# Kernel tuning notes

Measured on AMD Instinct MI355X. Metric: run time of the kernel, lower is better.

Reference implementation:

```python
import jax, jax.numpy as jnp
import numpy as np

NUM_HEADS = 8

def _qkv(t, W, b, H):
    # t: [B, L, C] -> q, k, v each [B, H, L, D]
    B, L, C = t.shape
    D = C // H
    qkv = (t @ W + b).reshape(B, L, 3, H, D)
    qkv = jnp.moveaxis(qkv, 2, 0)           # [3, B, L, H, D]
    qkv = jnp.swapaxes(qkv, 2, 3)           # [3, B, H, L, D]
    return qkv[0], qkv[1], qkv[2]

def _attend(q, k, v, scale):
    # q,k,v: [B, H, L, D] -> [B, L, C]
    B, H, L, D = q.shape
    scores = jnp.einsum('bhqd,bhkd->bhqk', q, k) * scale
    attn = jax.nn.softmax(scores, axis=-1)
    out = jnp.einsum('bhqk,bhkd->bhqd', attn, v)
    return jnp.swapaxes(out, 1, 2).reshape(B, L, H * D)

def setup_inputs() -> dict:
    key = jax.random.key(0)
    ks = jax.random.split(key, 7)
    B, N, C = 8, 2048, 512
    s_in = 1.0 / np.sqrt(C)
    return {
        'x': jax.random.normal(ks[0], (B, N, C), dtype=jnp.float32),
        'W_rgb_qkv': jax.random.normal(ks[1], (C, 3 * C), dtype=jnp.float32) * s_in,
        'b_rgb_qkv': jax.random.normal(ks[2], (3 * C,), dtype=jnp.float32) * 0.02,
        'W_depth_qkv': jax.random.normal(ks[3], (C, 3 * C), dtype=jnp.float32) * s_in,
        'b_depth_qkv': jax.random.normal(ks[4], (3 * C,), dtype=jnp.float32) * 0.02,
        'W_proj': jax.random.normal(ks[5], (C, C), dtype=jnp.float32) * s_in,
        'b_proj': jax.random.normal(ks[6], (C,), dtype=jnp.float32) * 0.02,
    }

def reference(x, W_rgb_qkv, b_rgb_qkv, W_depth_qkv, b_depth_qkv, W_proj, b_proj):
    B, N, C = x.shape
    H = NUM_HEADS
    D = C // H
    scale = D ** -0.5
    L = N // 2
    rgb, depth = x[:, :L], x[:, L:]
    rq, rk, rv = _qkv(rgb, W_rgb_qkv, b_rgb_qkv, H)
    dq, dk, dv = _qkv(depth, W_depth_qkv, b_depth_qkv, H)
    # rgb queries attend to depth K/V (named depth_v in torch code)
    depth_out = _attend(rq, dk, dv, scale)
    # depth queries attend to rgb K/V (named rgb_v in torch code)
    rgb_out = _attend(dq, rk, rv, scale)
    out = jnp.concatenate([rgb_out, depth_out], axis=1)  # [B, N, C]
    return out @ W_proj + b_proj
```

## Files before the change

kernel.cpp:

```cpp
#include <hip/hip_runtime.h>
#include <hip/hip_bf16.h>

typedef __attribute__((ext_vector_type(8))) short s16x8;
typedef __attribute__((ext_vector_type(4))) float f32x4;

__device__ __forceinline__ ushort f2bf(float f) {
  union { float f; unsigned int u; } c; c.f = f;
  unsigned int u = c.u + 0x7fffu + ((c.u >> 16) & 1u);
  return (ushort)(u >> 16);
}

__device__ __forceinline__ unsigned int pack2(float lo, float hi) {
  __hip_bfloat162 b2 = __float22bfloat162_rn(make_float2(lo, hi));
  union { __hip_bfloat162 b; unsigned int u; } c; c.b = b2;
  return c.u;
}

__device__ __forceinline__ s16x8 ld16(const ushort* p) {
  union { uint4 u; s16x8 s; } c;
  c.u = *reinterpret_cast<const uint4*>(p);
  return c.s;
}

__device__ __forceinline__ f32x4 mfma16(s16x8 a, s16x8 b, f32x4 c) {
  return __builtin_amdgcn_mfma_f32_16x16x32_bf16(a, b, c, 0, 0, 0);
}

__device__ __forceinline__ float exp2fast(float x) { return __builtin_amdgcn_exp2f(x); }

__device__ __forceinline__ void gld_lds16(const void* g, void* l) {
  __builtin_amdgcn_global_load_lds(
      (const __attribute__((address_space(1))) void*)g,
      (__attribute__((address_space(3))) void*)l, 16, 0, 0);
}


__global__ __launch_bounds__(256) void k_prep(
    const float* __restrict__ x, ushort* __restrict__ xb,
    const float* __restrict__ Wr, ushort* __restrict__ WtR,
    const float* __restrict__ Wd, ushort* __restrict__ WtD,
    const float* __restrict__ Wp, ushort* __restrict__ WtP) {
  __shared__ float tile[32][33];
  int b = blockIdx.x, t = threadIdx.x;
  if (b < 8192) {
    int i = (b * 256 + t) * 4;
    float4 v = *reinterpret_cast<const float4*>(x + i);
    ushort4 o;
    o.x = f2bf(v.x); o.y = f2bf(v.y); o.z = f2bf(v.z); o.w = f2bf(v.w);
    *reinterpret_cast<ushort4*>(xb + i) = o;
    return;
  }
  b -= 8192;
  const float* src; ushort* dst; int N;
  if (b < 768)      { src = Wr; dst = WtR; N = 1536; }
  else if (b < 1536){ b -= 768;  src = Wd; dst = WtD; N = 1536; }
  else              { b -= 1536; src = Wp; dst = WtP; N = 512; }
  int nb = N >> 5;
  int n0 = (b % nb) * 32, k0 = (b / nb) * 32;
  int tx = t & 31, ty = t >> 5;
#pragma unroll
  for (int i = 0; i < 32; i += 8)
    tile[ty + i][tx] = src[(k0 + ty + i) * N + (n0 + tx)];
  __syncthreads();
#pragma unroll
  for (int i = 0; i < 32; i += 8)
    dst[(size_t)(n0 + ty + i) * 512 + (k0 + tx)] = f2bf(tile[tx][ty + i]);
}


__device__ __forceinline__ s16x8 lds_frag(const char* lds, int row, int c) {
  union { uint4 u; s16x8 s; } cv;
  cv.u = *reinterpret_cast<const uint4*>(lds + row * 128 + ((c ^ (row & 7)) * 16));
  return cv.s;
}

__device__ __forceinline__ s16x8 lds_frag32(const char* lds, int row, int c) {
  union { uint4 u; s16x8 s; } cv;
  cv.u = *reinterpret_cast<const uint4*>(lds + row * 64 + ((c ^ ((row >> 1) & 3)) * 16));
  return cv.s;
}

__device__ __forceinline__ void stage_lds(const ushort* __restrict__ src, int ld,
                                          char* ldsbase, int t) {
#pragma unroll
  for (int p = 0; p < 4; ++p) {
    int chunk = p * 256 + t;
    int r = chunk >> 3, cc = chunk & 7;
    gld_lds16(src + r * ld + ((cc ^ (r & 7)) * 8), ldsbase + (chunk & ~63) * 16);
  }
}


template <bool TRANS>
__global__ __launch_bounds__(256) void k_qkv(
    const ushort* __restrict__ xb, const ushort* __restrict__ WtR,
    const ushort* __restrict__ WtD, const float* __restrict__ bR,
    const float* __restrict__ bD, ushort* __restrict__ Qb,
    ushort* __restrict__ Kb, ushort* __restrict__ Vt) {
  __shared__ __align__(16) char lds[49152];
  int m0 = blockIdx.x * 128;
  int n0 = (TRANS ? 1024 : 0) + blockIdx.y * 128;
  int s = m0 >> 13, bb = (m0 >> 10) & 7, lbase = m0 & 1023;
  const ushort* A = xb + (size_t)(bb * 2048 + s * 1024 + lbase) * 512;
  const ushort* Wt = (s ? WtD : WtR) + (size_t)n0 * 512;
  const float* bias = s ? bD : bR;
  int t = threadIdx.x;
  int wid = t >> 6, ln = t & 15, g = (t & 63) >> 4;
  int wr = wid >> 1, wc = wid & 1;

  int r0 = t >> 2, c0 = t & 3;
  int r1 = (t + 256) >> 2, c1 = t & 3;
  int so0 = r0 * 512 + ((c0 ^ ((r0 >> 1) & 3)) * 8);
  int so1 = r1 * 512 + ((c1 ^ ((r1 >> 1) & 3)) * 8);
  int ldu = (t & ~63) * 16;

  const ushort* As = A;
  const ushort* Bs = Wt;
  char* b0 = lds;
  char* b1 = lds + 16384;
  char* b2 = lds + 32768;

  f32x4 acc[4][4] = {};

  gld_lds16(As + so0, b0 + ldu);
  gld_lds16(As + so1, b0 + 4096 + ldu);
  gld_lds16(Bs + so0, b0 + 8192 + ldu);
  gld_lds16(Bs + so1, b0 + 12288 + ldu);
  As += 32; Bs += 32;
  gld_lds16(As + so0, b1 + ldu);
  gld_lds16(As + so1, b1 + 4096 + ldu);
  gld_lds16(Bs + so0, b1 + 8192 + ldu);
  gld_lds16(Bs + so1, b1 + 12288 + ldu);
  As += 32; Bs += 32;
  asm volatile("s_waitcnt vmcnt(4)" ::: "memory");
  __builtin_amdgcn_sched_barrier(0);
  __builtin_amdgcn_s_barrier();
  __builtin_amdgcn_sched_barrier(0);

  for (int ks = 0; ks < 16; ++ks) {
    if (ks < 14) {
      gld_lds16(As + so0, b2 + ldu);
      gld_lds16(As + so1, b2 + 4096 + ldu);
      gld_lds16(Bs + so0, b2 + 8192 + ldu);
      gld_lds16(Bs + so1, b2 + 12288 + ldu);
      As += 32; Bs += 32;
    }
    s16x8 af[4], bf[4];
    __builtin_amdgcn_s_setprio(1);
#pragma unroll
    for (int mi = 0; mi < 4; ++mi) af[mi] = lds_frag32(b0, wr * 64 + mi * 16 + ln, g);
#pragma unroll
    for (int ni = 0; ni < 4; ++ni) bf[ni] = lds_frag32(b0 + 8192, wc * 64 + ni * 16 + ln, g);
#pragma unroll
    for (int mi = 0; mi < 4; ++mi)
#pragma unroll
      for (int ni = 0; ni < 4; ++ni)
        acc[mi][ni] = TRANS ? mfma16(bf[ni], af[mi], acc[mi][ni])
                            : mfma16(af[mi], bf[ni], acc[mi][ni]);
    __builtin_amdgcn_s_setprio(0);

    if (ks < 15) {
      if (ks < 14) {
        asm volatile("s_waitcnt vmcnt(4)" ::: "memory");
      } else {
        asm volatile("s_waitcnt vmcnt(0)" ::: "memory");
      }
      __builtin_amdgcn_sched_barrier(0);
      __builtin_amdgcn_s_barrier();
      __builtin_amdgcn_sched_barrier(0);
    }
    char* tmp = b0; b0 = b1; b1 = b2; b2 = tmp;
  }

  int hb_base = (s * 8 + bb) * 8;
  if (!TRANS) {
    bool isK = (n0 >> 9) != 0;
    ushort* dst = isK ? Kb : Qb;
    float sc = isK ? 1.0f : 0.18033688011112042f;
#pragma unroll
    for (int mi = 0; mi < 4; ++mi)
#pragma unroll
      for (int ni = 0; ni < 4; ++ni) {
        f32x4 v = acc[mi][ni];
        int col = n0 + wc * 64 + ni * 16 + ln;
        int h = (col >> 6) & 7, d = col & 63;
        float bv = bias[col];
        ushort* hp = dst + ((size_t)(hb_base + h) << 16);
        int lr = lbase + wr * 64 + mi * 16 + g * 4;
#pragma unroll
        for (int j = 0; j < 4; ++j) hp[(lr + j) * 64 + d] = f2bf((v[j] + bv) * sc);
      }
  } else {
    __syncthreads();
    ushort* et = (ushort*)lds;
#pragma unroll
    for (int mi = 0; mi < 4; ++mi) {
      int ll = wr * 64 + mi * 16 + ln;
      int lpl = (ll & ~63) | (ll & 0x23) | ((ll & 0x0C) << 1) | ((ll & 0x10) >> 2);
      int chunk = lpl >> 3, within = lpl & 7;
#pragma unroll
      for (int ni = 0; ni < 4; ++ni) {
        f32x4 v = acc[mi][ni];
        int crb = wc * 64 + ni * 16 + g * 4;
#pragma unroll
        for (int j = 0; j < 4; ++j) {
          int cr = crb + j;
          float bv = bias[n0 + cr];
          *(ushort*)((char*)et + cr * 256 + ((chunk ^ (cr & 15)) * 16) + within * 2)
              = f2bf(v[j] + bv);
        }
      }
    }
    __syncthreads();
#pragma unroll
    for (int pass = 0; pass < 8; ++pass) {
      int rrow = pass * 16 + (t >> 4);
      int c16 = t & 15;
      int col = n0 + rrow;
      int h = (col >> 6) & 7, d = col & 63;
      uint4 vv = *(const uint4*)((const char*)et + rrow * 256 + ((c16 ^ (rrow & 15)) * 16));
      *reinterpret_cast<uint4*>(Vt + ((size_t)(hb_base + h) << 16) + d * 1024 + lbase + c16 * 8)
          = vv;
    }
  }
}


__global__ __launch_bounds__(512) void k_attn(const ushort* __restrict__ Qb,
                                              const ushort* __restrict__ Kb,
                                              const ushort* __restrict__ Vt,
                                              ushort* __restrict__ AO) {
  __shared__ __align__(16) char lds[32768];
  int bid = blockIdx.x;
  int set = bid & 127, qb = bid >> 7;
  int pair = set & 1, h = (set >> 1) & 7, bb = set >> 4;
  int sQ = 1 - pair, sKV = pair;
  const ushort* Qp = Qb + ((size_t)((sQ * 8 + bb) * 8 + h) << 16);
  const ushort* Kp = Kb + ((size_t)((sKV * 8 + bb) * 8 + h) << 16);
  const ushort* Vp = Vt + ((size_t)((sKV * 8 + bb) * 8 + h) << 16);
  int t = threadIdx.x, w = t >> 6, ln = t & 15, g = (t & 63) >> 4;
  int q0 = qb * 128 + w * 16;
  s16x8 qf0 = ld16(Qp + (q0 + ln) * 64 + g * 8);
  s16x8 qf1 = ld16(Qp + (q0 + ln) * 64 + 32 + g * 8);

  int r = t >> 3, cc = t & 7;
  int kof = r * 64 + ((cc ^ (r & 7)) * 8);
  int vof = r * 1024 + ((cc ^ (r & 7)) * 8);
  int ldst = (t & ~63) * 16;

  float ls = 0.f;
  f32x4 oc[4] = {};

  const ushort* kstage = Kp;
  const ushort* vstage = Vp;

  char* bc = lds;
  char* bn = lds + 16384;

  gld_lds16(kstage + kof, bc + ldst);
  gld_lds16(vstage + vof, bc + 8192 + ldst);
  kstage += 4096; vstage += 64;
  asm volatile("s_waitcnt vmcnt(0)" ::: "memory");
  __builtin_amdgcn_sched_barrier(0);
  __builtin_amdgcn_s_barrier();
  __builtin_amdgcn_sched_barrier(0);

  for (int it = 0; it < 16; ++it) {
    if (it < 15) {
      gld_lds16(kstage + kof, bn + ldst);
      gld_lds16(vstage + vof, bn + 8192 + ldst);
      kstage += 4096; vstage += 64;
    }

    f32x4 z[4];
    __builtin_amdgcn_s_setprio(1);
#pragma unroll
    for (int s = 0; s < 4; ++s) {
      s16x8 k0 = lds_frag(bc, s * 16 + ln, g);
      s16x8 k1 = lds_frag(bc, s * 16 + ln, 4 + g);
      f32x4 z1 = {}; z1 = mfma16(k0, qf0, z1); z1 = mfma16(k1, qf1, z1); z[s] = z1;
    }
    __builtin_amdgcn_s_setprio(0);

    unsigned int pw[8];
#pragma unroll
    for (int s = 0; s < 4; ++s) {
      float p0 = exp2fast(z[s][0]), p1 = exp2fast(z[s][1]);
      float p2 = exp2fast(z[s][2]), p3 = exp2fast(z[s][3]);
      ls += (p0 + p1) + (p2 + p3);
      pw[2 * s] = pack2(p0, p1); pw[2 * s + 1] = pack2(p2, p3);
    }
    union { uint4 u; s16x8 v; } c0, c1;
    c0.u = make_uint4(pw[0], pw[1], pw[2], pw[3]);
    c1.u = make_uint4(pw[4], pw[5], pw[6], pw[7]);
    s16x8 pf0 = c0.v, pf1 = c1.v;

    __builtin_amdgcn_s_setprio(1);
#pragma unroll
    for (int d = 0; d < 4; ++d) {
      s16x8 v0 = lds_frag(bc + 8192, d * 16 + ln, g);
      s16x8 v1 = lds_frag(bc + 8192, d * 16 + ln, 4 + g);
      oc[d] = mfma16(v0, pf0, oc[d]);
      oc[d] = mfma16(v1, pf1, oc[d]);
    }
    __builtin_amdgcn_s_setprio(0);

    if (it < 15) {
      asm volatile("s_waitcnt vmcnt(0)" ::: "memory");
      __builtin_amdgcn_sched_barrier(0);
      __builtin_amdgcn_s_barrier();
      __builtin_amdgcn_sched_barrier(0);
    }
    char* tmp = bc; bc = bn; bn = tmp;
  }

  ls += __shfl_xor(ls, 16, 64);
  ls += __shfl_xor(ls, 32, 64);
  float inv = 1.0f / ls;
  int orow = bb * 2048 + pair * 1024 + q0 + ln;
#pragma unroll
  for (int d = 0; d < 4; ++d) {
    uint2 st;
    st.x = pack2(oc[d][0] * inv, oc[d][1] * inv);
    st.y = pack2(oc[d][2] * inv, oc[d][3] * inv);
    *reinterpret_cast<uint2*>(AO + (size_t)orow * 512 + h * 64 + d * 16 + 4 * g) = st;
  }
}


__global__ __launch_bounds__(256) void k_gemm_proj(const ushort* __restrict__ AO,
                                                   const ushort* __restrict__ WtP,
                                                   const float* __restrict__ bP,
                                                   float* __restrict__ Out) {
  __shared__ __align__(16) char lds[65536];
  int m0 = blockIdx.x * 128, n0 = blockIdx.y * 128;
  const ushort* A = AO + (size_t)m0 * 512;
  const ushort* Wt = WtP + (size_t)n0 * 512;
  int t = threadIdx.x;
  int wid = t >> 6, ln = t & 15, g = (t & 63) >> 4;
  int wr = wid >> 1, wc = wid & 1;
  f32x4 acc[4][4] = {};
  stage_lds(A, 512, lds, t);
  stage_lds(Wt, 512, lds + 16384, t);
  __syncthreads();
  for (int ks = 0; ks < 8; ++ks) {
    char* cbuf = lds + (ks & 1) * 32768;
    if (ks < 7) {
      char* nbuf = lds + ((ks + 1) & 1) * 32768;
      stage_lds(A + (ks + 1) * 64, 512, nbuf, t);
      stage_lds(Wt + (ks + 1) * 64, 512, nbuf + 16384, t);
    }
    char* ldsA = cbuf;
    char* ldsB = cbuf + 16384;
#pragma unroll
    for (int kk = 0; kk < 2; ++kk) {
      s16x8 af[4], bf[4];
#pragma unroll
      for (int mi = 0; mi < 4; ++mi) af[mi] = lds_frag(ldsA, wr * 64 + mi * 16 + ln, kk * 4 + g);
#pragma unroll
      for (int ni = 0; ni < 4; ++ni) bf[ni] = lds_frag(ldsB, wc * 64 + ni * 16 + ln, kk * 4 + g);
#pragma unroll
      for (int mi = 0; mi < 4; ++mi)
#pragma unroll
        for (int ni = 0; ni < 4; ++ni) acc[mi][ni] = mfma16(af[mi], bf[ni], acc[mi][ni]);
    }
    __syncthreads();
  }
#pragma unroll
  for (int mi = 0; mi < 4; ++mi)
#pragma unroll
    for (int ni = 0; ni < 4; ++ni) {
      f32x4 v = acc[mi][ni];
      int col = n0 + wc * 64 + ni * 16 + ln;
      float bv = bP[col];
      int r0 = m0 + wr * 64 + mi * 16 + g * 4;
#pragma unroll
      for (int j = 0; j < 4; ++j) Out[(size_t)(r0 + j) * 512 + col] = v[j] + bv;
    }
}


extern "C" void kernel_launch(void* const* d_in, const int* in_sizes, int n_in,
                              void* d_out, int out_size, void* d_ws, size_t ws_size,
                              hipStream_t stream) {
  const float* x      = (const float*)d_in[0];
  const float* W_rgb  = (const float*)d_in[1];
  const float* b_rgb  = (const float*)d_in[2];
  const float* W_dep  = (const float*)d_in[3];
  const float* b_dep  = (const float*)d_in[4];
  const float* W_proj = (const float*)d_in[5];
  const float* b_proj = (const float*)d_in[6];
  float* out = (float*)d_out;

  char* ws = (char*)d_ws;
  ushort* xb  = (ushort*)(ws + 0);
  ushort* WtR = (ushort*)(ws + 16777216);
  ushort* WtD = (ushort*)(ws + 18350080);
  ushort* WtP = (ushort*)(ws + 19922944);
  ushort* Qb  = (ushort*)(ws + 20447232);
  ushort* Kb  = (ushort*)(ws + 37224448);
  ushort* Vt  = (ushort*)(ws + 54001664);
  ushort* AO  = (ushort*)(ws + 70778880);

  k_prep<<<9984, 256, 0, stream>>>(x, xb, W_rgb, WtR, W_dep, WtD, W_proj, WtP);
  k_qkv<false><<<dim3(128, 8), 256, 0, stream>>>(xb, WtR, WtD, b_rgb, b_dep, Qb, Kb, Vt);
  k_qkv<true><<<dim3(128, 4), 256, 0, stream>>>(xb, WtR, WtD, b_rgb, b_dep, Qb, Kb, Vt);
  k_attn<<<1024, 512, 0, stream>>>(Qb, Kb, Vt, AO);
  k_gemm_proj<<<dim3(128, 4), 256, 0, stream>>>(AO, WtP, b_proj, out);
}
```

Before: 131.6 us.

## Process two 16-row query tiles per wave in attention kernel with half the threads

The attention kernel now launches 256 threads per block instead of 512, and each wave handles 32 query rows as two 16-row MFMA tiles. Each K and V fragment read from LDS is reused for both tiles, and each thread issues two global-to-LDS loads per matrix to cover the 64-row staging tile. The goal is to halve LDS fragment traffic per query row and amortize staging and barrier overhead across more MFMA work. In exchange, register use per thread roughly doubles and there are fewer waves per block, which could reduce latency hiding.

```diff
diff --git a/kernel.cpp b/kernel.cpp
--- a/kernel.cpp
+++ b/kernel.cpp
@@ -226,7 +226,7 @@
 }
 
 
-__global__ __launch_bounds__(512) void k_attn(const ushort* __restrict__ Qb,
+__global__ __launch_bounds__(256) void k_attn(const ushort* __restrict__ Qb,
                                               const ushort* __restrict__ Kb,
                                               const ushort* __restrict__ Vt,
                                               ushort* __restrict__ AO) {
@@ -239,17 +239,22 @@
   const ushort* Kp = Kb + ((size_t)((sKV * 8 + bb) * 8 + h) << 16);
   const ushort* Vp = Vt + ((size_t)((sKV * 8 + bb) * 8 + h) << 16);
   int t = threadIdx.x, w = t >> 6, ln = t & 15, g = (t & 63) >> 4;
-  int q0 = qb * 128 + w * 16;
-  s16x8 qf0 = ld16(Qp + (q0 + ln) * 64 + g * 8);
-  s16x8 qf1 = ld16(Qp + (q0 + ln) * 64 + 32 + g * 8);
-
-  int r = t >> 3, cc = t & 7;
-  int kof = r * 64 + ((cc ^ (r & 7)) * 8);
-  int vof = r * 1024 + ((cc ^ (r & 7)) * 8);
+  int q0 = qb * 128 + w * 32;
+  s16x8 qf0a = ld16(Qp + (q0 + ln) * 64 + g * 8);
+  s16x8 qf1a = ld16(Qp + (q0 + ln) * 64 + 32 + g * 8);
+  s16x8 qf0b = ld16(Qp + (q0 + 16 + ln) * 64 + g * 8);
+  s16x8 qf1b = ld16(Qp + (q0 + 16 + ln) * 64 + 32 + g * 8);
+
+  int rA = t >> 3, ccA = t & 7;
+  int rB = 32 + (t >> 3), ccB = t & 7;
+  int kofA = rA * 64 + ((ccA ^ (rA & 7)) * 8);
+  int kofB = rB * 64 + ((ccB ^ (rB & 7)) * 8);
+  int vofA = rA * 1024 + ((ccA ^ (rA & 7)) * 8);
+  int vofB = rB * 1024 + ((ccB ^ (rB & 7)) * 8);
   int ldst = (t & ~63) * 16;
 
-  float ls = 0.f;
-  f32x4 oc[4] = {};
+  float ls_a = 0.f, ls_b = 0.f;
+  f32x4 oca[4] = {}, ocb[4] = {};
 
   const ushort* kstage = Kp;
   const ushort* vstage = Vp;
@@ -257,8 +262,10 @@
   char* bc = lds;
   char* bn = lds + 16384;
 
-  gld_lds16(kstage + kof, bc + ldst);
-  gld_lds16(vstage + vof, bc + 8192 + ldst);
+  gld_lds16(kstage + kofA, bc + ldst);
+  gld_lds16(kstage + kofB, bc + 4096 + ldst);
+  gld_lds16(vstage + vofA, bc + 8192 + ldst);
+  gld_lds16(vstage + vofB, bc + 12288 + ldst);
   kstage += 4096; vstage += 64;
   asm volatile("s_waitcnt vmcnt(0)" ::: "memory");
   __builtin_amdgcn_sched_barrier(0);
@@ -267,41 +274,52 @@
 
   for (int it = 0; it < 16; ++it) {
     if (it < 15) {
-      gld_lds16(kstage + kof, bn + ldst);
-      gld_lds16(vstage + vof, bn + 8192 + ldst);
+      gld_lds16(kstage + kofA, bn + ldst);
+      gld_lds16(kstage + kofB, bn + 4096 + ldst);
+      gld_lds16(vstage + vofA, bn + 8192 + ldst);
+      gld_lds16(vstage + vofB, bn + 12288 + ldst);
       kstage += 4096; vstage += 64;
     }
 
-    f32x4 z[4];
+    f32x4 za[4], zb[4];
     __builtin_amdgcn_s_setprio(1);
 #pragma unroll
     for (int s = 0; s < 4; ++s) {
       s16x8 k0 = lds_frag(bc, s * 16 + ln, g);
       s16x8 k1 = lds_frag(bc, s * 16 + ln, 4 + g);
-      f32x4 z1 = {}; z1 = mfma16(k0, qf0, z1); z1 = mfma16(k1, qf1, z1); z[s] = z1;
+      f32x4 z1 = {}; z1 = mfma16(k0, qf0a, z1); z1 = mfma16(k1, qf1a, z1); za[s] = z1;
+      f32x4 z2 = {}; z2 = mfma16(k0, qf0b, z2); z2 = mfma16(k1, qf1b, z2); zb[s] = z2;
     }
     __builtin_amdgcn_s_setprio(0);
 
-    unsigned int pw[8];
+    unsigned int pwa[8], pwb[8];
 #pragma unroll
     for (int s = 0; s < 4; ++s) {
-      float p0 = exp2fast(z[s][0]), p1 = exp2fast(z[s][1]);
-      float p2 = exp2fast(z[s][2]), p3 = exp2fast(z[s][3]);
-      ls += (p0 + p1) + (p2 + p3);
-      pw[2 * s] = pack2(p0, p1); pw[2 * s + 1] = pack2(p2, p3);
-    }
-    union { uint4 u; s16x8 v; } c0, c1;
-    c0.u = make_uint4(pw[0], pw[1], pw[2], pw[3]);
-    c1.u = make_uint4(pw[4], pw[5], pw[6], pw[7]);
-    s16x8 pf0 = c0.v, pf1 = c1.v;
+      float p0 = exp2fast(za[s][0]), p1 = exp2fast(za[s][1]);
+      float p2 = exp2fast(za[s][2]), p3 = exp2fast(za[s][3]);
+      ls_a += (p0 + p1) + (p2 + p3);
+      pwa[2 * s] = pack2(p0, p1); pwa[2 * s + 1] = pack2(p2, p3);
+      float r0 = exp2fast(zb[s][0]), r1 = exp2fast(zb[s][1]);
+      float r2 = exp2fast(zb[s][2]), r3 = exp2fast(zb[s][3]);
+      ls_b += (r0 + r1) + (r2 + r3);
+      pwb[2 * s] = pack2(r0, r1); pwb[2 * s + 1] = pack2(r2, r3);
+    }
+    union { uint4 u; s16x8 v; } c0, c1, c2, c3;
+    c0.u = make_uint4(pwa[0], pwa[1], pwa[2], pwa[3]);
+    c1.u = make_uint4(pwa[4], pwa[5], pwa[6], pwa[7]);
+    c2.u = make_uint4(pwb[0], pwb[1], pwb[2], pwb[3]);
+    c3.u = make_uint4(pwb[4], pwb[5], pwb[6], pwb[7]);
+    s16x8 pf0a = c0.v, pf1a = c1.v, pf0b = c2.v, pf1b = c3.v;
 
     __builtin_amdgcn_s_setprio(1);
 #pragma unroll
     for (int d = 0; d < 4; ++d) {
       s16x8 v0 = lds_frag(bc + 8192, d * 16 + ln, g);
       s16x8 v1 = lds_frag(bc + 8192, d * 16 + ln, 4 + g);
-      oc[d] = mfma16(v0, pf0, oc[d]);
-      oc[d] = mfma16(v1, pf1, oc[d]);
+      oca[d] = mfma16(v0, pf0a, oca[d]);
+      oca[d] = mfma16(v1, pf1a, oca[d]);
+      ocb[d] = mfma16(v0, pf0b, ocb[d]);
+      ocb[d] = mfma16(v1, pf1b, ocb[d]);
     }
     __builtin_amdgcn_s_setprio(0);
 
@@ -314,16 +332,22 @@
     char* tmp = bc; bc = bn; bn = tmp;
   }
 
-  ls += __shfl_xor(ls, 16, 64);
-  ls += __shfl_xor(ls, 32, 64);
-  float inv = 1.0f / ls;
+  ls_a += __shfl_xor(ls_a, 16, 64);
+  ls_a += __shfl_xor(ls_a, 32, 64);
+  ls_b += __shfl_xor(ls_b, 16, 64);
+  ls_b += __shfl_xor(ls_b, 32, 64);
+  float inva = 1.0f / ls_a, invb = 1.0f / ls_b;
   int orow = bb * 2048 + pair * 1024 + q0 + ln;
 #pragma unroll
   for (int d = 0; d < 4; ++d) {
     uint2 st;
-    st.x = pack2(oc[d][0] * inv, oc[d][1] * inv);
-    st.y = pack2(oc[d][2] * inv, oc[d][3] * inv);
+    st.x = pack2(oca[d][0] * inva, oca[d][1] * inva);
+    st.y = pack2(oca[d][2] * inva, oca[d][3] * inva);
     *reinterpret_cast<uint2*>(AO + (size_t)orow * 512 + h * 64 + d * 16 + 4 * g) = st;
+    uint2 st2;
+    st2.x = pack2(ocb[d][0] * invb, ocb[d][1] * invb);
+    st2.y = pack2(ocb[d][2] * invb, ocb[d][3] * invb);
+    *reinterpret_cast<uint2*>(AO + (size_t)(orow + 16) * 512 + h * 64 + d * 16 + 4 * g) = st2;
   }
 }
 
@@ -405,6 +429,6 @@
   k_prep<<<9984, 256, 0, stream>>>(x, xb, W_rgb, WtR, W_dep, WtD, W_proj, WtP);
   k_qkv<false><<<dim3(128, 8), 256, 0, stream>>>(xb, WtR, WtD, b_rgb, b_dep, Qb, Kb, Vt);
   k_qkv<true><<<dim3(128, 4), 256, 0, stream>>>(xb, WtR, WtD, b_rgb, b_dep, Qb, Kb, Vt);
-  k_attn<<<1024, 512, 0, stream>>>(Qb, Kb, Vt, AO);
+  k_attn<<<1024, 256, 0, stream>>>(Qb, Kb, Vt, AO);
   k_gemm_proj<<<dim3(128, 4), 256, 0, stream>>>(AO, WtP, b_proj, out);
 }
```

Result: no change. 132.4 us (+0.6%).
